# Performance work log

Measured on AMD Instinct MI355X. Metric: run time of the kernel, lower is better.

## Reference

```python
import jax, jax.numpy as jnp
import numpy as np

LAMBDA_TEMPORAL = 0.5
LAMBDA_IDENTITY = 0.1
EPS = 1e-6


def setup_inputs() -> dict:
    key = jax.random.key(0)
    k1, k2, k3 = jax.random.split(key, 3)
    B, T, N = 16, 256, 2048
    pred_tracks_3d = jax.random.normal(k1, (B, T, N, 3), dtype=jnp.float32)
    gt_tracks_3d = jax.random.normal(k2, (B, T, N, 3), dtype=jnp.float32)
    gt_visibility = jax.random.uniform(k3, (B, T, N), dtype=jnp.float32)
    return {
        'pred_tracks_3d': pred_tracks_3d,
        'gt_tracks_3d': gt_tracks_3d,
        'gt_visibility': gt_visibility,
    }


def _compute_losses(pred, gt, vis):
    # visibility mask (B, T, N)
    m = (vis > 0.5).astype(pred.dtype)
    num_visible = jnp.sum(m)

    coord_w = jnp.array([1.0, 1.0, 2.0], dtype=pred.dtype)
    weighted_sq = jnp.square(pred - gt) * coord_w  # (B,T,N,3)
    recon = jnp.where(
        num_visible > 0,
        jnp.sum(weighted_sq * m[..., None]) / jnp.maximum(num_visible, 1.0),
        0.0,
    )

    # --- temporal: masked velocity MSE (visible in both adjacent frames) ---
    pred_vel = pred[:, 1:] - pred[:, :-1]
    gt_vel = gt[:, 1:] - gt[:, :-1]
    vel_mask = m[:, 1:] * m[:, :-1]  # (B,T-1,N)
    num_vel = jnp.sum(vel_mask)
    temporal = jnp.where(
        num_vel > 0,
        jnp.sum(jnp.square(pred_vel - gt_vel) * vel_mask[..., None]) / jnp.maximum(num_vel, 1.0),
        0.0,
    )

    # --- identity: per-point unbiased variance ratio over visible (b,t) samples ---
    n = jnp.sum(m, axis=(0, 1))  # (N,) visible count per point

    def masked_var(x):
        # unbiased (ddof=1) per-point, per-coord variance over masked (B,T) entries
        mean = jnp.einsum('btn,btnc->nc', m, x) / jnp.maximum(n, 1.0)[:, None]
        ss = jnp.einsum('btn,btnc->nc', m, jnp.square(x - mean[None, None]))
        return ss / jnp.maximum(n - 1.0, 1.0)[:, None]  # (N,3)

    pred_var = masked_var(pred)
    gt_var = masked_var(gt)
    var_ratio = jnp.sum(jnp.abs(pred_var - gt_var), axis=1) / (jnp.sum(gt_var, axis=1) + EPS)
    num_points = pred.shape[2]
    identity = jnp.sum(jnp.where(n > 1, var_ratio, 0.0)) / num_points

    # --- adaptive re-weighting (no-grad in original) ---
    rl = jax.lax.stop_gradient(recon)
    tl = jax.lax.stop_gradient(temporal)
    il = jax.lax.stop_gradient(identity)
    all_pos = (rl > 0) & (tl > 0) & (il > 0)
    max_comp = jnp.maximum(jnp.maximum(rl, tl), il)
    target = max_comp / 3.0
    thresh = 10.0 * target

    def adjust(base, comp):
        return jnp.where(all_pos & (comp > thresh), base * target / jnp.maximum(comp, 1e-30), base)

    rec_w = adjust(1.0, rl)
    temp_w = adjust(LAMBDA_TEMPORAL, tl)
    id_w = adjust(LAMBDA_IDENTITY, il)

    total = rec_w * recon + temp_w * temporal + id_w * identity
    return jnp.stack([total, recon, temporal, identity])


def reference(pred_tracks_3d, gt_tracks_3d, gt_visibility):
    # returns [total_loss, reconstruction_loss, temporal_loss, identity_loss]
    return _compute_losses(pred_tracks_3d, gt_tracks_3d, gt_visibility)
```

## Files before the change

kernel.cpp:

```cpp
#include <hip/hip_runtime.h>

#define BB 16
#define TT 256
#define NN 2048
#define TC 32
#define WSBASE 16


__device__ __forceinline__ float waveReduceSum(float v) {
#pragma unroll
  for (int o = 32; o > 0; o >>= 1) v += __shfl_down(v, o, 64);
  return v;
}

__global__ __launch_bounds__(256) void stats_kernel(
    const float* __restrict__ pred, const float* __restrict__ gt,
    const float* __restrict__ vis, float* __restrict__ ws) {
  const int n  = blockIdx.x * 256 + threadIdx.x;
  const int b  = blockIdx.y;
  const int t0 = blockIdx.z * TC;
  const int tstart = (t0 == 0) ? 0 : t0 - 1;

  float cnt = 0.f;
  float sp0 = 0, sp1 = 0, sp2 = 0, qp0 = 0, qp1 = 0, qp2 = 0;
  float sg0 = 0, sg1 = 0, sg2 = 0, qg0 = 0, qg1 = 0, qg2 = 0;
  float recon = 0, temporal = 0, nvel = 0;
  float pm = 0, pp0 = 0, pp1 = 0, pp2 = 0, pg0 = 0, pg1 = 0, pg2 = 0;

  for (int t = tstart; t < t0 + TC; ++t) {
    size_t idx = ((size_t)(b * TT + t) * NN + n);
    float v = vis[idx];
    float m = (v > 0.5f) ? 1.f : 0.f;
    size_t i3 = idx * 3;
    float a0 = pred[i3 + 0], a1 = pred[i3 + 1], a2 = pred[i3 + 2];
    float g0 = gt[i3 + 0],  g1 = gt[i3 + 1],  g2 = gt[i3 + 2];

    if (t >= t0) {
      cnt += m;
      sp0 += m * a0; sp1 += m * a1; sp2 += m * a2;
      qp0 += m * a0 * a0; qp1 += m * a1 * a1; qp2 += m * a2 * a2;
      sg0 += m * g0; sg1 += m * g1; sg2 += m * g2;
      qg0 += m * g0 * g0; qg1 += m * g1 * g1; qg2 += m * g2 * g2;
      float d0 = a0 - g0, d1 = a1 - g1, d2 = a2 - g2;
      recon += m * (d0 * d0 + d1 * d1 + 2.f * d2 * d2);
    }
    if (t > tstart) {
      float mv = m * pm;
      float vx = (a0 - pp0) - (g0 - pg0);
      float vy = (a1 - pp1) - (g1 - pg1);
      float vz = (a2 - pp2) - (g2 - pg2);
      temporal += mv * (vx * vx + vy * vy + vz * vz);
      nvel += mv;
    }
    pm = m; pp0 = a0; pp1 = a1; pp2 = a2; pg0 = g0; pg1 = g1; pg2 = g2;
  }

  float* pts = ws + WSBASE;
  atomicAdd(&pts[0 * NN + n], cnt);
  atomicAdd(&pts[1 * NN + n], sp0);
  atomicAdd(&pts[2 * NN + n], sp1);
  atomicAdd(&pts[3 * NN + n], sp2);
  atomicAdd(&pts[4 * NN + n], qp0);
  atomicAdd(&pts[5 * NN + n], qp1);
  atomicAdd(&pts[6 * NN + n], qp2);
  atomicAdd(&pts[7 * NN + n], sg0);
  atomicAdd(&pts[8 * NN + n], sg1);
  atomicAdd(&pts[9 * NN + n], sg2);
  atomicAdd(&pts[10 * NN + n], qg0);
  atomicAdd(&pts[11 * NN + n], qg1);
  atomicAdd(&pts[12 * NN + n], qg2);

  __shared__ float sred[3][4];
  float r0 = waveReduceSum(recon);
  float r1 = waveReduceSum(temporal);
  float r2 = waveReduceSum(nvel);
  int lane = threadIdx.x & 63, w = threadIdx.x >> 6;
  if (lane == 0) { sred[0][w] = r0; sred[1][w] = r1; sred[2][w] = r2; }
  __syncthreads();
  if (threadIdx.x < 3) {
    float s = sred[threadIdx.x][0] + sred[threadIdx.x][1] +
              sred[threadIdx.x][2] + sred[threadIdx.x][3];
    atomicAdd(&ws[threadIdx.x], s);
  }
}

__global__ __launch_bounds__(256) void identity_kernel(float* __restrict__ ws) {
  const int n = blockIdx.x * 256 + threadIdx.x;
  const float* pts = ws + WSBASE;
  float c   = pts[0 * NN + n];
  float sp0 = pts[1 * NN + n], sp1 = pts[2 * NN + n], sp2 = pts[3 * NN + n];
  float qp0 = pts[4 * NN + n], qp1 = pts[5 * NN + n], qp2 = pts[6 * NN + n];
  float sg0 = pts[7 * NN + n], sg1 = pts[8 * NN + n], sg2 = pts[9 * NN + n];
  float qg0 = pts[10 * NN + n], qg1 = pts[11 * NN + n], qg2 = pts[12 * NN + n];

  float inv = 1.f / fmaxf(c, 1.f);
  float dv  = 1.f / fmaxf(c - 1.f, 1.f);
  float pv0 = (qp0 - sp0 * sp0 * inv) * dv;
  float pv1 = (qp1 - sp1 * sp1 * inv) * dv;
  float pv2 = (qp2 - sp2 * sp2 * inv) * dv;
  float gv0 = (qg0 - sg0 * sg0 * inv) * dv;
  float gv1 = (qg1 - sg1 * sg1 * inv) * dv;
  float gv2 = (qg2 - sg2 * sg2 * inv) * dv;

  float num = fabsf(pv0 - gv0) + fabsf(pv1 - gv1) + fabsf(pv2 - gv2);
  float den = gv0 + gv1 + gv2 + 1e-6f;
  float contrib = (c > 1.f) ? (num / den) : 0.f;

  __shared__ float sred[2][4];
  float r0 = waveReduceSum(contrib);
  float r1 = waveReduceSum(c);
  int lane = threadIdx.x & 63, w = threadIdx.x >> 6;
  if (lane == 0) { sred[0][w] = r0; sred[1][w] = r1; }
  __syncthreads();
  if (threadIdx.x < 2) {
    float s = sred[threadIdx.x][0] + sred[threadIdx.x][1] +
              sred[threadIdx.x][2] + sred[threadIdx.x][3];
    atomicAdd(&ws[3 + threadIdx.x], s);
  }
}

__global__ void finalize_kernel(const float* __restrict__ ws, float* __restrict__ out) {
  float nv = ws[4];
  float recon = (nv > 0.f) ? ws[0] / fmaxf(nv, 1.f) : 0.f;
  float nvel = ws[2];
  float temporal = (nvel > 0.f) ? ws[1] / fmaxf(nvel, 1.f) : 0.f;
  float identity = ws[3] / (float)NN;

  float rl = recon, tl = temporal, il = identity;
  bool all_pos = (rl > 0.f) && (tl > 0.f) && (il > 0.f);
  float maxc = fmaxf(rl, fmaxf(tl, il));
  float target = maxc / 3.f;
  float thresh = 10.f * target;
  float rw = (all_pos && rl > thresh) ? 1.0f * target / fmaxf(rl, 1e-30f) : 1.0f;
  float tw = (all_pos && tl > thresh) ? 0.5f * target / fmaxf(tl, 1e-30f) : 0.5f;
  float iw = (all_pos && il > thresh) ? 0.1f * target / fmaxf(il, 1e-30f) : 0.1f;

  out[0] = rw * recon + tw * temporal + iw * identity;
  out[1] = recon;
  out[2] = temporal;
  out[3] = identity;
}

extern "C" void kernel_launch(void* const* d_in, const int* in_sizes, int n_in,
                              void* d_out, int out_size, void* d_ws, size_t ws_size,
                              hipStream_t stream) {
  const float* pred = (const float*)d_in[0];
  const float* gt   = (const float*)d_in[1];
  const float* vis  = (const float*)d_in[2];
  float* out = (float*)d_out;
  float* ws  = (float*)d_ws;

  hipMemsetAsync(d_ws, 0, (WSBASE + 13 * NN) * sizeof(float), stream);

  dim3 g1(NN / 256, BB, TT / TC);
  stats_kernel<<<g1, 256, 0, stream>>>(pred, gt, vis, ws);
  identity_kernel<<<dim3(NN / 256), 256, 0, stream>>>(ws);
  finalize_kernel<<<1, 1, 0, stream>>>(ws, out);
}
```

Measured before the change: 257.2 us.

## Halve time chunks, unroll with float3 loads, and slice per-point atomics

Halves the time chunk per block, which doubles the grid, and fully unrolls the loop with float3 loads through precomputed base pointers. Per-point atomic accumulators are spread over 8 workspace slices indexed by batch to reduce atomic contention, and the identity kernel sums the slices. A launch-bounds occupancy hint is added. The cost is a larger memset, more atomics overall, and more halo frames re-read because chunks are shorter.

After: 254.2 us. No clear change (-1.1%).

```diff
diff --git a/kernel.cpp b/kernel.cpp
--- a/kernel.cpp
+++ b/kernel.cpp
@@ -3,7 +3,8 @@
 #define BB 16
 #define TT 256
 #define NN 2048
-#define TC 32
+#define TC 16
+#define NSLICE 8
 #define WSBASE 16
 
 
@@ -13,49 +14,59 @@
   return v;
 }
 
-__global__ __launch_bounds__(256) void stats_kernel(
+__global__ __launch_bounds__(256, 8) void stats_kernel(
     const float* __restrict__ pred, const float* __restrict__ gt,
     const float* __restrict__ vis, float* __restrict__ ws) {
   const int n  = blockIdx.x * 256 + threadIdx.x;
   const int b  = blockIdx.y;
   const int t0 = blockIdx.z * TC;
-  const int tstart = (t0 == 0) ? 0 : t0 - 1;
+
+  const size_t frame0 = (size_t)(b * TT + t0) * NN + n;
+  const float3* __restrict__ pp = (const float3*)pred + frame0;
+  const float3* __restrict__ gp = (const float3*)gt + frame0;
+  const float*  __restrict__ vp = vis + frame0;
 
   float cnt = 0.f;
   float sp0 = 0, sp1 = 0, sp2 = 0, qp0 = 0, qp1 = 0, qp2 = 0;
   float sg0 = 0, sg1 = 0, sg2 = 0, qg0 = 0, qg1 = 0, qg2 = 0;
   float recon = 0, temporal = 0, nvel = 0;
-  float pm = 0, pp0 = 0, pp1 = 0, pp2 = 0, pg0 = 0, pg1 = 0, pg2 = 0;
 
-  for (int t = tstart; t < t0 + TC; ++t) {
-    size_t idx = ((size_t)(b * TT + t) * NN + n);
-    float v = vis[idx];
-    float m = (v > 0.5f) ? 1.f : 0.f;
-    size_t i3 = idx * 3;
-    float a0 = pred[i3 + 0], a1 = pred[i3 + 1], a2 = pred[i3 + 2];
-    float g0 = gt[i3 + 0],  g1 = gt[i3 + 1],  g2 = gt[i3 + 2];
-
-    if (t >= t0) {
-      cnt += m;
-      sp0 += m * a0; sp1 += m * a1; sp2 += m * a2;
-      qp0 += m * a0 * a0; qp1 += m * a1 * a1; qp2 += m * a2 * a2;
-      sg0 += m * g0; sg1 += m * g1; sg2 += m * g2;
-      qg0 += m * g0 * g0; qg1 += m * g1 * g1; qg2 += m * g2 * g2;
-      float d0 = a0 - g0, d1 = a1 - g1, d2 = a2 - g2;
-      recon += m * (d0 * d0 + d1 * d1 + 2.f * d2 * d2);
-    }
-    if (t > tstart) {
-      float mv = m * pm;
-      float vx = (a0 - pp0) - (g0 - pg0);
-      float vy = (a1 - pp1) - (g1 - pg1);
-      float vz = (a2 - pp2) - (g2 - pg2);
-      temporal += mv * (vx * vx + vy * vy + vz * vz);
-      nvel += mv;
-    }
-    pm = m; pp0 = a0; pp1 = a1; pp2 = a2; pg0 = g0; pg1 = g1; pg2 = g2;
+  float3 ppv, pgv;
+  float mprev;
+  {
+    const long off = (t0 == 0) ? 0 : -(long)NN;
+    ppv = pp[off];
+    pgv = gp[off];
+    float v = vp[off];
+    mprev = (t0 != 0 && v > 0.5f) ? 1.f : 0.f;
   }
 
-  float* pts = ws + WSBASE;
+#pragma unroll
+  for (int i = 0; i < TC; ++i) {
+    float3 a = pp[(size_t)i * NN];
+    float3 g = gp[(size_t)i * NN];
+    float v = vp[(size_t)i * NN];
+    float m = (v > 0.5f) ? 1.f : 0.f;
+
+    cnt += m;
+    sp0 += m * a.x; sp1 += m * a.y; sp2 += m * a.z;
+    qp0 += m * a.x * a.x; qp1 += m * a.y * a.y; qp2 += m * a.z * a.z;
+    sg0 += m * g.x; sg1 += m * g.y; sg2 += m * g.z;
+    qg0 += m * g.x * g.x; qg1 += m * g.y * g.y; qg2 += m * g.z * g.z;
+    float d0 = a.x - g.x, d1 = a.y - g.y, d2 = a.z - g.z;
+    recon += m * (d0 * d0 + d1 * d1 + 2.f * d2 * d2);
+
+    float mv = m * mprev;
+    float vx = (a.x - ppv.x) - (g.x - pgv.x);
+    float vy = (a.y - ppv.y) - (g.y - pgv.y);
+    float vz = (a.z - ppv.z) - (g.z - pgv.z);
+    temporal += mv * (vx * vx + vy * vy + vz * vz);
+    nvel += mv;
+
+    ppv = a; pgv = g; mprev = m;
+  }
+
+  float* pts = ws + WSBASE + (size_t)(b & (NSLICE - 1)) * 13 * NN;
   atomicAdd(&pts[0 * NN + n], cnt);
   atomicAdd(&pts[1 * NN + n], sp0);
   atomicAdd(&pts[2 * NN + n], sp1);
@@ -86,12 +97,21 @@
 
 __global__ __launch_bounds__(256) void identity_kernel(float* __restrict__ ws) {
   const int n = blockIdx.x * 256 + threadIdx.x;
-  const float* pts = ws + WSBASE;
-  float c   = pts[0 * NN + n];
-  float sp0 = pts[1 * NN + n], sp1 = pts[2 * NN + n], sp2 = pts[3 * NN + n];
-  float qp0 = pts[4 * NN + n], qp1 = pts[5 * NN + n], qp2 = pts[6 * NN + n];
-  float sg0 = pts[7 * NN + n], sg1 = pts[8 * NN + n], sg2 = pts[9 * NN + n];
-  float qg0 = pts[10 * NN + n], qg1 = pts[11 * NN + n], qg2 = pts[12 * NN + n];
+  const float* base = ws + WSBASE;
+  float st[13];
+#pragma unroll
+  for (int k = 0; k < 13; ++k) st[k] = 0.f;
+#pragma unroll
+  for (int s = 0; s < NSLICE; ++s) {
+    const float* pts = base + (size_t)s * 13 * NN;
+#pragma unroll
+    for (int k = 0; k < 13; ++k) st[k] += pts[k * NN + n];
+  }
+  float c = st[0];
+  float sp0 = st[1], sp1 = st[2], sp2 = st[3];
+  float qp0 = st[4], qp1 = st[5], qp2 = st[6];
+  float sg0 = st[7], sg1 = st[8], sg2 = st[9];
+  float qg0 = st[10], qg1 = st[11], qg2 = st[12];
 
   float inv = 1.f / fmaxf(c, 1.f);
   float dv  = 1.f / fmaxf(c - 1.f, 1.f);
@@ -150,7 +170,7 @@
   float* out = (float*)d_out;
   float* ws  = (float*)d_ws;
 
-  hipMemsetAsync(d_ws, 0, (WSBASE + 13 * NN) * sizeof(float), stream);
+  hipMemsetAsync(d_ws, 0, (WSBASE + (size_t)NSLICE * 13 * NN) * sizeof(float), stream);
 
   dim3 g1(NN / 256, BB, TT / TC);
   stats_kernel<<<g1, 256, 0, stream>>>(pred, gt, vis, ws);
```
